# Performance work log

Hardware: AMD Instinct MI355X
Metric: run time of the kernel (lower is better)

The kernel has to match this reference:

```python
import jax, jax.numpy as jnp
import numpy as np

B, N, D_FEAT = 16, 1024, 64
NPOINT, RADIUS, NSAMPLE = 512, 0.2, 32
EPS = 1e-5


def _square_distance(src, dst):
    # src [b,S,3], dst [b,N,3] -> [b,S,N]
    d = -2.0 * jnp.einsum('bsc,bnc->bsn', src, dst)
    d = d + jnp.sum(src * src, -1)[:, :, None]
    d = d + jnp.sum(dst * dst, -1)[:, None, :]
    return d


def _fps(xyz, npoint):
    # xyz [b,N,3] -> indices [b,npoint]; seeded by point farthest from the mean
    b, n, _ = xyz.shape
    centroid = jnp.mean(xyz, axis=1, keepdims=True)
    distance = jnp.minimum(jnp.full((b, n), 1e10, xyz.dtype),
                           jnp.sum((xyz - centroid) ** 2, -1))
    farthest = jnp.argmax(distance, -1)
    bidx = jnp.arange(b)

    def body(carry, _):
        dist, far = carry
        c = xyz[bidx[:, None], far[:, None]]  # [b,1,3]
        dist = jnp.minimum(dist, jnp.sum((xyz - c) ** 2, -1))
        return (dist, jnp.argmax(dist, -1)), far

    _, idx = jax.lax.scan(body, (distance, farthest), None, length=npoint)
    return idx.T  # [b, npoint]


def _gather(points, idx):
    # points [b,N,C], idx [b,...] -> [b,...,C]
    return jax.vmap(lambda p, i: p[i])(points, idx)


def _query_ball(radius, nsample, xyz, new_xyz):
    # faithful to torch: mask out-of-radius with N, full sort, take first nsample,
    # replace sentinels by the first (closest-index) in-ball point
    b, n, _ = xyz.shape
    sqr = _square_distance(new_xyz, xyz)  # [b,S,N]
    idx = jnp.where(sqr > radius ** 2, n, jnp.arange(n)[None, None, :])
    idx = jnp.sort(idx, axis=-1)[:, :, :nsample]
    first = idx[:, :, :1]
    return jnp.where(idx == n, first, idx)


def _qbn(x):
    # QBN_RM training mode: divide by per-channel RMS of detached activations
    mean = jnp.mean(jax.lax.stop_gradient(x) ** 2, axis=(0, 2, 3))
    return x / jnp.sqrt(mean + EPS)[None, :, None, None]


def _qrelu(x):
    # scale each 3-vector by mod / max(mod, 1), coefficient detached
    b3, c, s, k = x.shape
    b = b3 // 3
    xd = jax.lax.stop_gradient(x).reshape(b, 3, c, s, k)
    mod = jnp.sqrt(jnp.sum(xd * xd, axis=1))  # [b,c,s,k]
    coeff = mod / jnp.maximum(mod, 1.0)
    return jnp.broadcast_to(coeff[:, None], (b, 3, c, s, k)).reshape(b3, c, s, k) * x


def _qmaxpool(x):
    # our_mpool1d with kernel (1, nsample): pick the max-modulus sample over K,
    # gather the same index for all 3 quaternion components
    b3, c, s, k = x.shape
    b = b3 // 3
    x5 = x.reshape(b, 3, c, s, k)
    mod = jnp.sum(jax.lax.stop_gradient(x5) ** 2, axis=1)  # argmax of mod == argmax of mod^2
    idx = jnp.argmax(mod, axis=-1)  # [b,c,s]
    idxb = jnp.broadcast_to(idx[:, None, :, :, None], (b, 3, c, s, 1))
    y = jnp.take_along_axis(x5, idxb, axis=-1)[..., 0]  # [b,3,c,s]
    return y.reshape(b3, c, s)


def setup_inputs() -> dict:
    key = jax.random.key(0)
    k1, k2, k3, k4, k5 = jax.random.split(key, 5)
    xyz = jax.random.normal(k1, (B, 3, N), dtype=jnp.float32)
    points = jax.random.normal(k2, (B * 3, D_FEAT, N), dtype=jnp.float32)
    W0 = jax.random.normal(k3, (64, 66), dtype=jnp.float32) * np.sqrt(2.0 / 66)
    W1 = jax.random.normal(k4, (64, 64), dtype=jnp.float32) * np.sqrt(2.0 / 64)
    W2 = jax.random.normal(k5, (128, 64), dtype=jnp.float32) * np.sqrt(2.0 / 64)
    return {"xyz": xyz, "points": points, "W0": W0, "W1": W1, "W2": W2}


def reference(xyz, points, W0, W1, W2):
    xyz_t = xyz.transpose(0, 2, 1)      # [B,N,3]
    pts_t = points.transpose(0, 2, 1)   # [B*3,N,D]

    fps_idx = _fps(xyz_t, NPOINT)                       # [B,S]
    new_xyz = _gather(xyz_t, fps_idx)                   # [B,S,3]
    idx = _query_ball(RADIUS, NSAMPLE, xyz_t, new_xyz)  # [B,S,K]

    g_xyz = _gather(xyz_t, idx)                         # [B,S,K,3]
    g_norm = g_xyz - new_xyz[:, :, None, :]
    gx = g_xyz.transpose(0, 3, 1, 2).reshape(B * 3, NPOINT, NSAMPLE, 1)
    gn = g_norm.transpose(0, 3, 1, 2).reshape(B * 3, NPOINT, NSAMPLE, 1)
    idx3 = jnp.broadcast_to(idx[:, None], (B, 3, NPOINT, NSAMPLE)).reshape(B * 3, NPOINT, NSAMPLE)
    gp = _gather(pts_t, idx3)                           # [B*3,S,K,D]

    x = jnp.concatenate([gn, gx, gp], axis=-1)          # [B*3,S,K,D+2]
    x = x.transpose(0, 3, 1, 2)                         # [B*3,D+2,S,K]
    for W in (W0, W1, W2):
        x = jnp.einsum('bcsk,oc->bosk', x, W)           # 1x1 conv, no bias
        x = _qrelu(_qbn(x))
    new_feat = _qmaxpool(x)                             # [B*3,128,S]
    return new_xyz.transpose(0, 2, 1), new_feat
```

## Files before the change

### kernel.cpp

```cpp
#include <hip/hip_runtime.h>

typedef unsigned int u32;
typedef unsigned long long u64;
typedef float v2f __attribute__((ext_vector_type(2)));

#define NB 16
#define NPT 1024
#define NP 512
#define NS 32
#define DF 64
#define RAD2 0.04f
#define EPSQ 1e-5f
#define CNTF 786432.0f
#define NGRP 8192
#define TCAP 96
#define TSLOT 128
#define NTILE_MAX 2731
#define NBALLBLK 4096
#define NFILLBLK 1366

__device__ __forceinline__ float rmul(float a, float b){ return __fmul_rn(a,b); }
__device__ __forceinline__ float radd(float a, float b){ return __fadd_rn(a,b); }
__device__ __forceinline__ float sq3(float a, float b, float c){
  return radd(radd(rmul(a,a), rmul(b,b)), rmul(c,c));
}

__device__ __forceinline__ float wave_sum64(float v){
  #pragma unroll
  for(int m=1;m<64;m<<=1) v += __shfl_xor(v, m, 64);
  return v;
}
__device__ __forceinline__ float half_sum32(float v){
  #pragma unroll
  for(int m=1;m<32;m<<=1) v += __shfl_xor(v, m, 64);
  return v;
}

#define DPPK(CTRL) do{ \
  unsigned _lo = (unsigned)k, _hi = (unsigned)(k>>32); \
  unsigned _mlo = (unsigned)__builtin_amdgcn_mov_dpp((int)_lo, (CTRL), 0xF, 0xF, true); \
  unsigned _mhi = (unsigned)__builtin_amdgcn_mov_dpp((int)_hi, (CTRL), 0xF, 0xF, true); \
  u64 _mk = ((u64)_mhi<<32) | _mlo; \
  k = (_mk > k) ? _mk : k; \
}while(0)

template<int PT>
__global__ __launch_bounds__(256, 1) void fps_combo(const float* __restrict__ xyz,
                                                    float* __restrict__ out0,
                                                    const float* __restrict__ pts,
                                                    float* __restrict__ ptsT,
                                                    u32* __restrict__ witem,
                                                    int* __restrict__ idxb_full,
                                                    int* __restrict__ cnt_full,
                                                    int* __restrict__ farIdx){
#pragma clang fp contract(off)
  const int bid = blockIdx.x;
  const int t = threadIdx.x;

  if(bid >= 8){
    if(bid < 8 + NBALLBLK){
      const int row = (bid - 8)*4 + (t>>6);
      const int lane = t & 63;
      const int b = row >> 10;
      const int nc = row & 1023;
      const float* xb = xyz + b*3*NPT;
      const float s0 = xb[nc], s1 = xb[NPT+nc], s2 = xb[2*NPT+nc];
      const float ss = sq3(s0,s1,s2);
      int base = 0;
      int* rowp = idxb_full + row*NS;
      for(int chk=0; chk<16 && base<NS; ++chk){
        const int n = chk*64 + lane;
        float d0 = xb[n], d1 = xb[NPT+n], d2 = xb[2*NPT+n];
        float dd = sq3(d0,d1,d2);
        float p  = radd(radd(rmul(s0,d0), rmul(s1,d1)), rmul(s2,d2));
        float sqr = radd(radd(rmul(-2.0f,p), ss), dd);
        bool inc = !(sqr > RAD2);
        u64 mask = __ballot(inc);
        if(inc){
          int slot = base + __popcll(mask & ((1ull<<lane)-1ull));
          if(slot < NS) rowp[slot] = n;
        }
        base += __popcll(mask);
      }
      if(lane==0) cnt_full[row] = (base < NS) ? base : NS;
    } else {
      const int gid = (bid - 8 - NBALLBLK)*256 + t;
      if(gid < NTILE_MAX*TSLOT) witem[gid] = 0xFFFFFFFFu;
      if constexpr(PT){
        const int w = gid >> 6, ln = gid & 63;
        if(w < 48*16){
          const int b3 = w >> 4, n0 = (w & 15) << 6;
          const float* src = pts + (((size_t)b3*64 + ln) << 10);
          float* dst = ptsT + (((size_t)b3*1024 + n0) << 6) + ln;
          #pragma unroll 4
          for(int i=0;i<64;i++) dst[(size_t)i << 6] = src[n0 + i];
        }
      }
    }
    return;
  }

  __shared__ float4 plds[2048];
  if(t >= 64) return;
  __builtin_amdgcn_s_setprio(3);
  const int lane = t;
  const int half = lane >> 5;
  const int hl   = lane & 31;
  const int b    = 2*bid + half;
  const float* xb = xyz + b*3*NPT;

  v2f px2[16], py2[16], pz2[16], dist2[16];
  u32 loj[32];
  #pragma unroll
  for(int i=0;i<16;i++){
    const int n0 = 64*i + hl, n1 = n0 + 32;
    float x0v = xb[n0],        x1v = xb[n1];
    float y0v = xb[NPT+n0],    y1v = xb[NPT+n1];
    float z0v = xb[2*NPT+n0],  z1v = xb[2*NPT+n1];
    px2[i].x = x0v; px2[i].y = x1v;
    py2[i].x = y0v; py2[i].y = y1v;
    pz2[i].x = z0v; pz2[i].y = z1v;
    loj[2*i]   = 1023u - (u32)n0;
    loj[2*i+1] = 1023u - (u32)n1;
    plds[(half<<10) + n0] = make_float4(x0v, y0v, z0v, 0.f);
    plds[(half<<10) + n1] = make_float4(x1v, y1v, z1v, 0.f);
  }
  float sx=0.f, sy=0.f, sz=0.f;
  #pragma unroll
  for(int i=0;i<16;i++){
    sx += px2[i].x; sx += px2[i].y;
    sy += py2[i].x; sy += py2[i].y;
    sz += pz2[i].x; sz += pz2[i].y;
  }
  sx = half_sum32(sx); sy = half_sum32(sy); sz = half_sum32(sz);
  const float cx = sx/1024.f, cy = sy/1024.f, cz = sz/1024.f;
  {
    v2f cx2; cx2.x=cx; cx2.y=cx;
    v2f cy2; cy2.x=cy; cy2.y=cy;
    v2f cz2; cz2.x=cz; cz2.y=cz;
    #pragma unroll
    for(int i=0;i<16;i++){
      v2f dx = px2[i]-cx2, dy = py2[i]-cy2, dz = pz2[i]-cz2;
      v2f m1 = dx*dx, m2 = dy*dy, a1 = m1+m2, m3 = dz*dz, s2 = a1+m3;
      dist2[i].x = fminf(1e10f, s2.x);
      dist2[i].y = fminf(1e10f, s2.y);
    }
  }
  auto reduce2 = [&](int& fA, int& fB){
    u64 kk[16];
    #pragma unroll
    for(int i=0;i<16;i++){
      float a = dist2[i].x, bb = dist2[i].y;
      bool tk = bb > a;
      float dw = tk ? bb : a;
      u32   lw = tk ? loj[2*i+1] : loj[2*i];
      kk[i] = ((u64)__float_as_uint(dw)<<32) | lw;
    }
    #pragma unroll
    for(int i=0;i<8;i++){ u64 l=kk[2*i], r=kk[2*i+1]; kk[i] = (r>l)?r:l; }
    #pragma unroll
    for(int i=0;i<4;i++){ u64 l=kk[2*i], r=kk[2*i+1]; kk[i] = (r>l)?r:l; }
    #pragma unroll
    for(int i=0;i<2;i++){ u64 l=kk[2*i], r=kk[2*i+1]; kk[i] = (r>l)?r:l; }
    u64 k = (kk[1]>kk[0]) ? kk[1] : kk[0];
    DPPK(0xB1); DPPK(0x4E); DPPK(0x124); DPPK(0x128); DPPK(0x142);
    unsigned lo = (unsigned)k;
    fA = 1023 - __builtin_amdgcn_readlane((int)lo, 31);
    fB = 1023 - __builtin_amdgcn_readlane((int)lo, 63);
  };

  __asm__ volatile("s_waitcnt lgkmcnt(0)" ::: "memory");
  int farA, farB;
  reduce2(farA, farB);
  for(int it=0; it<NP; ++it){
    const int farv = (lane & 32) ? farB : farA;
    const float4 qv = plds[(half<<10) + farv];
    if(hl == 0){
      out0[(b*3+0)*NP + it] = qv.x;
      out0[(b*3+1)*NP + it] = qv.y;
      out0[(b*3+2)*NP + it] = qv.z;
      farIdx[b*NP + it] = farv;
    }
    v2f qx2; qx2.x=qv.x; qx2.y=qv.x;
    v2f qy2; qy2.x=qv.y; qy2.y=qv.y;
    v2f qz2; qz2.x=qv.z; qz2.y=qv.z;
    #pragma unroll
    for(int i=0;i<16;i++){
      v2f dx = px2[i]-qx2, dy = py2[i]-qy2, dz = pz2[i]-qz2;
      v2f m1 = dx*dx, m2 = dy*dy, a1 = m1+m2, m3 = dz*dz, s2 = a1+m3;
      dist2[i].x = fminf(dist2[i].x, s2.x);
      dist2[i].y = fminf(dist2[i].y, s2.y);
    }
    reduce2(farA, farB);
  }
}

__global__ __launch_bounds__(1024) void pack_kernel(const int* __restrict__ farIdx,
                                                    const int* __restrict__ cnt_full,
                                                    const int* __restrict__ idxb_full,
                                                    u32* __restrict__ witem,
                                                    int* __restrict__ ntile_dev,
                                                    int* __restrict__ cntb){
  const int t = threadIdx.x;
  const int lane = t & 63;
  const int wv = t >> 6;
  int c[8]; int rowid[8]; int s0 = 0;
  #pragma unroll
  for(int i=0;i<8;i++){
    const int g = t*8+i;
    const int far = farIdx[g];
    rowid[i] = ((g>>9)<<10) + far;
    c[i] = cnt_full[rowid[i]];
    cntb[g] = c[i];
    s0 += c[i];
  }
  int pre = s0;
  #pragma unroll
  for(int d=1; d<64; d<<=1){
    int v = __shfl_up(pre, d, 64);
    if(lane >= d) pre += v;
  }
  __shared__ int wsum[16];
  if(lane==63) wsum[wv] = pre;
  __syncthreads();
  int wo = 0;
  #pragma unroll
  for(int w=0;w<16;w++) if(w < wv) wo += wsum[w];
  int m = wo + pre - s0;
  if(t==1023) *ntile_dev = (wo + pre + TCAP - 1) / TCAP;
  #pragma unroll
  for(int i=0;i<8;i++){
    const int g = t*8+i; const int cc = c[i];
    const int tile = m / TCAP; const int slot = m - TCAP*tile;
    const int* rp = idxb_full + rowid[i]*NS;
    for(int j=0;j<cc;j++){
      witem[tile*TSLOT + slot + j] = (u32)((g<<15) | (j<<10) | rp[j]);
    }
    m += cc;
  }
}

template<int DEPTH, int PT>
__global__ __launch_bounds__(384) void pass_kernel(
  const float* __restrict__ xyz, const float* __restrict__ ptsrc,
  const float* __restrict__ W0, const float* __restrict__ W1, const float* __restrict__ W2,
  const float* __restrict__ out0, const u32* __restrict__ witem,
  const int* __restrict__ cntb, const int* __restrict__ ntile_dev,
  const float* __restrict__ inv1, const float* __restrict__ inv2,
  float* __restrict__ part, float* __restrict__ out1,
  int cache_tiles, float* __restrict__ cacheA, float* __restrict__ cacheB)
{
  const int t = threadIdx.x;
  const int c3 = t >> 7;
  const int r  = t & 127;
  const int lane = t & 63;
  const int wv = t >> 6;
  const int bi = blockIdx.x;

  if(bi >= *ntile_dev) return;
  const bool use_cache = (bi < cache_tiles);
  float* cslotA = cacheA + ((size_t)bi*TSLOT + r)*192 + (size_t)c3*64;
  float* cslotB = cacheB + ((size_t)bi*TSLOT + r)*192 + (size_t)c3*64;

  __shared__ float sq[3][128][17];
  __shared__ float wstat[6][128];
  for(int i=t; i<6*128; i+=384) (&wstat[0][0])[i] = 0.f;
  __syncthreads();

  const u32 w = witem[bi*TSLOT + r];
  const bool valid = (w != 0xFFFFFFFFu);
  const int bs = valid ? (int)(w >> 15) : 0;
  const int j  = valid ? (int)((w >> 10) & 31) : 1;
  const int n  = valid ? (int)(w & 1023) : 0;
  const int b = bs >> 9;
  const int s = bs & 511;
  const int b3 = b*3 + c3;
  const int cv = cntb[bs];
  const float wgt = valid ? ((j==0) ? (float)(33 - cv) : 1.0f) : 0.0f;

  float acc2[64];
  const bool skip01 = (DEPTH == 3) && use_cache;

  if(!skip01){
    float acc64[64];
    if(DEPTH >= 2 && use_cache){
      #pragma unroll
      for(int q=0;q<16;q++){
        float4 v = ((const float4*)cslotA)[q];
        acc64[4*q]=v.x; acc64[4*q+1]=v.y; acc64[4*q+2]=v.z; acc64[4*q+3]=v.w;
      }
    } else {
      const float gx = xyz[b3*NPT + n];
      const float cx = out0[b3*NP + s];
      float x0[66];
      x0[0] = gx - cx;
      x0[1] = gx;
      if constexpr(PT){
        const float4* pr4 = reinterpret_cast<const float4*>(ptsrc + (((size_t)b3<<10) + (size_t)n)*DF);
        #pragma unroll
        for(int q=0;q<16;q++){
          float4 v = pr4[q];
          x0[2+4*q] = v.x; x0[3+4*q] = v.y; x0[4+4*q] = v.z; x0[5+4*q] = v.w;
        }
      } else {
        const float* pr = ptsrc + ((size_t)b3*DF)*NPT + n;
        #pragma unroll
        for(int c=0;c<DF;c++) x0[2+c] = pr[(size_t)c*NPT];
      }
      #pragma unroll
      for(int ch=0; ch<4; ++ch){
        #pragma unroll
        for(int oo=0;oo<16;oo++){
          const int o = ch*16+oo;
          float a = 0.f;
          #pragma unroll
          for(int c=0;c<66;c++) a = fmaf(W0[o*66+c], x0[c], a);
          acc64[o] = a;
        }
      }
      if(DEPTH == 1 && use_cache){
        #pragma unroll
        for(int q=0;q<16;q++){
          float4 v; v.x=acc64[4*q]; v.y=acc64[4*q+1]; v.z=acc64[4*q+2]; v.w=acc64[4*q+3];
          ((float4*)cslotA)[q] = v;
        }
      }
    }

    if constexpr(DEPTH == 1){
      #pragma unroll
      for(int o=0;o<64;o++){
        float v = wave_sum64(acc64[o]*acc64[o]*wgt);
        if(lane==0) wstat[wv][o] += v;
      }
      __syncthreads();
      if(t < 64){
        float sv = 0.f;
        #pragma unroll
        for(int wq=0;wq<6;wq++) sv += wstat[wq][t];
        part[bi*64 + t] = sv;
      }
      return;
    }

    float y1[64];
    #pragma unroll
    for(int ch=0; ch<4; ++ch){
      float xp16[16];
      #pragma unroll
      for(int oo=0;oo<16;oo++){
        const int o = ch*16+oo;
        float xp = acc64[o] * inv1[o];
        xp16[oo] = xp;
        sq[c3][r][oo] = xp*xp;
      }
      __syncthreads();
      #pragma unroll
      for(int oo=0;oo<16;oo++){
        float m2 = (sq[0][r][oo] + sq[1][r][oo]) + sq[2][r][oo];
        float mod = sqrtf(m2);
        float cf = (mod >= 1.f) ? 1.f : mod;
        y1[ch*16+oo] = cf * xp16[oo];
      }
      __syncthreads();
    }

    #pragma unroll
    for(int ch=0; ch<4; ++ch){
      #pragma unroll
      for(int oo=0;oo<16;oo++){
        const int o = ch*16+oo;
        float a = 0.f;
        #pragma unroll
        for(int c=0;c<64;c++) a = fmaf(W1[o*64+c], y1[c], a);
        acc2[o] = a;
      }
    }
    if(DEPTH == 2 && use_cache){
      #pragma unroll
      for(int q=0;q<16;q++){
        float4 v; v.x=acc2[4*q]; v.y=acc2[4*q+1]; v.z=acc2[4*q+2]; v.w=acc2[4*q+3];
        ((float4*)cslotB)[q] = v;
      }
    }
  } else {
    #pragma unroll
    for(int q=0;q<16;q++){
      float4 v = ((const float4*)cslotB)[q];
      acc2[4*q]=v.x; acc2[4*q+1]=v.y; acc2[4*q+2]=v.z; acc2[4*q+3]=v.w;
    }
  }

  if constexpr(DEPTH == 2){
    #pragma unroll
    for(int o=0;o<64;o++){
      float v = wave_sum64(acc2[o]*acc2[o]*wgt);
      if(lane==0) wstat[wv][o] += v;
    }
    __syncthreads();
    if(t < 64){
      float sv = 0.f;
      #pragma unroll
      for(int wq=0;wq<6;wq++) sv += wstat[wq][t];
      part[bi*64 + t] = sv;
    }
    return;
  }

  if constexpr(DEPTH == 3){
    float y2[64];
    #pragma unroll
    for(int ch=0; ch<4; ++ch){
      float xp16[16];
      #pragma unroll
      for(int oo=0;oo<16;oo++){
        const int o = ch*16+oo;
        float xp = acc2[o] * inv2[o];
        xp16[oo] = xp;
        sq[c3][r][oo] = xp*xp;
      }
      __syncthreads();
      #pragma unroll
      for(int oo=0;oo<16;oo++){
        float m2 = (sq[0][r][oo] + sq[1][r][oo]) + sq[2][r][oo];
        float mod = sqrtf(m2);
        float cf = (mod >= 1.f) ? 1.f : mod;
        y2[ch*16+oo] = cf * xp16[oo];
      }
      __syncthreads();
    }

    #pragma unroll
    for(int ch=0; ch<8; ++ch){
      #pragma unroll
      for(int oo=0;oo<16;oo++){
        const int o = ch*16+oo;
        float a = 0.f;
        #pragma unroll
        for(int c=0;c<64;c++) a = fmaf(W2[o*64+c], y2[c], a);
        sq[c3][r][oo] = a;
      }
      __syncthreads();
      if(c3 == 0){
        #pragma unroll
        for(int oo=0;oo<16;oo++){
          float a0 = sq[0][r][oo], a1 = sq[1][r][oo], a2 = sq[2][r][oo];
          float m2 = radd(radd(rmul(a0,a0), rmul(a1,a1)), rmul(a2,a2));
          float v = wave_sum64(m2*wgt);
          if(lane==0) wstat[wv][ch*16+oo] += v;
          if(valid && j==0){
            float bvv = m2; int bjj = 0;
            for(int jj=1; jj<cv; ++jj){
              float c0 = sq[0][r+jj][oo], c1 = sq[1][r+jj][oo], c2 = sq[2][r+jj][oo];
              float mm = radd(radd(rmul(c0,c0), rmul(c1,c1)), rmul(c2,c2));
              if(mm > bvv){ bvv = mm; bjj = jj; }
            }
            const int o = ch*16+oo;
            #pragma unroll
            for(int cc=0;cc<3;cc++){
              out1[(((size_t)(3*b+cc))*128 + o)*NP + s] = sq[cc][r+bjj][oo];
            }
          }
        }
      }
      __syncthreads();
    }
    if(t < 128){
      part[bi*128 + t] = wstat[0][t] + wstat[1][t];
    }
  }
}

__global__ __launch_bounds__(256) void fin_kernel(const float* __restrict__ part,
                                                  const int* __restrict__ ntile_dev, int nch,
                                                  float* __restrict__ inv){
  const int o = blockIdx.x;
  const int t = threadIdx.x;
  const int nblk = *ntile_dev;
  float sum = 0.f;
  for(int i=t; i<nblk; i+=256) sum += part[(size_t)i*nch + o];
  sum = wave_sum64(sum);
  __shared__ float red[4];
  if((t&63)==0) red[t>>6] = sum;
  __syncthreads();
  if(t==0){
    float tot = (red[0]+red[1])+(red[2]+red[3]);
    inv[o] = 1.0f / sqrtf(tot/CNTF + EPSQ);
  }
}

__global__ __launch_bounds__(256) void fin3_scale(const float* __restrict__ part3,
                                                  const int* __restrict__ ntile_dev,
                                                  float* __restrict__ out){
  const int o = blockIdx.x;
  const int t = threadIdx.x;
  const int nblk = *ntile_dev;
  float sum = 0.f;
  for(int i=t; i<nblk; i+=256) sum += part3[(size_t)i*128 + o];
  sum = wave_sum64(sum);
  __shared__ float red[4];
  __shared__ float sinv;
  if((t&63)==0) red[t>>6] = sum;
  __syncthreads();
  if(t==0){
    float tot = (red[0]+red[1])+(red[2]+red[3]);
    sinv = 1.0f / sqrtf(tot/CNTF + EPSQ);
  }
  __syncthreads();
  const float iv = sinv;
  float* base = out + NB*3*NP;
  const size_t str = (size_t)128*NP;
  for(int idx=t; idx<NB*NP; idx+=256){
    const int b = idx >> 9, s = idx & 511;
    size_t i0 = ((size_t)(b*3)*128 + o)*NP + s;
    float a0 = base[i0] * iv;
    float a1 = base[i0+str] * iv;
    float a2 = base[i0+2*str] * iv;
    float m2 = (a0*a0 + a1*a1) + a2*a2;
    float mod = sqrtf(m2);
    float cf = (mod >= 1.f) ? 1.f : mod;
    base[i0] = cf*a0; base[i0+str] = cf*a1; base[i0+2*str] = cf*a2;
  }
}

extern "C" void kernel_launch(void* const* d_in, const int* in_sizes, int n_in,
                              void* d_out, int out_size, void* d_ws, size_t ws_size,
                              hipStream_t stream){
  const float* xyz = (const float*)d_in[0];
  const float* pts = (const float*)d_in[1];
  const float* W0  = (const float*)d_in[2];
  const float* W1  = (const float*)d_in[3];
  const float* W2  = (const float*)d_in[4];
  float* out = (float*)d_out;

  char* p = (char*)d_ws;
  auto carve = [&](size_t bytes)->char*{
    char* q = p; p += (bytes + 255) & ~(size_t)255; return q;
  };
  int*   idxb_full = (int*)  carve((size_t)NB*NPT*NS*4);
  int*   cnt_full  = (int*)  carve((size_t)NB*NPT*4);
  int*   farIdx    = (int*)  carve((size_t)NGRP*4);
  int*   cntb      = (int*)  carve((size_t)NGRP*4);
  u32*   witem     = (u32*)  carve((size_t)NTILE_MAX*TSLOT*4);
  int*   ntile_dev = (int*)  carve(256);
  float* part1     = (float*)carve((size_t)NTILE_MAX*64*4);
  float* part2     = (float*)carve((size_t)NTILE_MAX*64*4);
  float* part3     = (float*)carve((size_t)NTILE_MAX*128*4);
  float* inv1      = (float*)carve(64*4);
  float* inv2      = (float*)carve(64*4);
  size_t base_need = (size_t)(p - (char*)d_ws);
  float* ptsT      = (float*)p;
  const size_t pt_bytes = (size_t)48*1024*64*4;
  const bool use_pt = (ws_size >= base_need + pt_bytes + (1u<<20));

  size_t fixed = base_need + (use_pt ? pt_bytes : 0);
  const size_t per_tile = (size_t)TSLOT*192*4*2;
  int cache_tiles = 0;
  if(ws_size > fixed + per_tile)
    cache_tiles = (int)((ws_size - fixed) / per_tile);
  if(cache_tiles > NTILE_MAX) cache_tiles = NTILE_MAX;
  float* cacheA = (float*)((char*)d_ws + fixed);
  float* cacheB = cacheA + (size_t)cache_tiles*TSLOT*192;

  float* out1 = out + NB*3*NP;
  const int nblk = 8 + NBALLBLK + NFILLBLK;

  if(use_pt) fps_combo<1><<<nblk, 256, 0, stream>>>(xyz, out, pts, ptsT, witem, idxb_full, cnt_full, farIdx);
  else       fps_combo<0><<<nblk, 256, 0, stream>>>(xyz, out, pts, nullptr, witem, idxb_full, cnt_full, farIdx);

  pack_kernel<<<1, 1024, 0, stream>>>(farIdx, cnt_full, idxb_full, witem, ntile_dev, cntb);

  if(use_pt){
    pass_kernel<1,1><<<NTILE_MAX, 384, 0, stream>>>(xyz, ptsT, W0, W1, W2, out, witem, cntb, ntile_dev, nullptr, nullptr, part1, nullptr, cache_tiles, cacheA, cacheB);
    fin_kernel<<<64, 256, 0, stream>>>(part1, ntile_dev, 64, inv1);
    pass_kernel<2,1><<<NTILE_MAX, 384, 0, stream>>>(xyz, ptsT, W0, W1, W2, out, witem, cntb, ntile_dev, inv1, nullptr, part2, nullptr, cache_tiles, cacheA, cacheB);
    fin_kernel<<<64, 256, 0, stream>>>(part2, ntile_dev, 64, inv2);
    pass_kernel<3,1><<<NTILE_MAX, 384, 0, stream>>>(xyz, ptsT, W0, W1, W2, out, witem, cntb, ntile_dev, inv1, inv2, part3, out1, cache_tiles, cacheA, cacheB);
  } else {
    pass_kernel<1,0><<<NTILE_MAX, 384, 0, stream>>>(xyz, pts, W0, W1, W2, out, witem, cntb, ntile_dev, nullptr, nullptr, part1, nullptr, cache_tiles, cacheA, cacheB);
    fin_kernel<<<64, 256, 0, stream>>>(part1, ntile_dev, 64, inv1);
    pass_kernel<2,0><<<NTILE_MAX, 384, 0, stream>>>(xyz, pts, W0, W1, W2, out, witem, cntb, ntile_dev, inv1, nullptr, part2, nullptr, cache_tiles, cacheA, cacheB);
    fin_kernel<<<64, 256, 0, stream>>>(part2, ntile_dev, 64, inv2);
    pass_kernel<3,0><<<NTILE_MAX, 384, 0, stream>>>(xyz, pts, W0, W1, W2, out, witem, cntb, ntile_dev, inv1, inv2, part3, out1, cache_tiles, cacheA, cacheB);
  }
  fin3_scale<<<128, 256, 0, stream>>>(part3, ntile_dev, out);
}
```

Before: 744.5 us.

## Fuse pack stage into FPS kernel via atomic completion flag; persistent pass grid

Removes the separate single-block pack kernel launch. An extra block is appended to the FPS/ball-query kernel that spins on a global atomic counter until all other blocks have signalled completion, then does the prefix-sum packing itself. The pass kernels also switch from one block per tile to a fixed 512-block grid that loops over tiles. The spin-wait relies on the last block being scheduled after the others and includes a timeout escape that could silently produce wrong results. A memset launch is added to reset the flag.

After: 958.6 us. 28.8% more time.

```diff
diff --git a/kernel.cpp b/kernel.cpp
--- a/kernel.cpp
+++ b/kernel.cpp
@@ -18,6 +18,8 @@
 #define NTILE_MAX 2731
 #define NBALLBLK 4096
 #define NFILLBLK 1366
+#define NSIG (8 + NBALLBLK + NFILLBLK)
+#define NPGRID 512
 
 __device__ __forceinline__ float rmul(float a, float b){ return __fmul_rn(a,b); }
 __device__ __forceinline__ float radd(float a, float b){ return __fadd_rn(a,b); }
@@ -43,6 +45,10 @@
   u64 _mk = ((u64)_mhi<<32) | _mlo; \
   k = (_mk > k) ? _mk : k; \
 }while(0)
+
+__device__ __forceinline__ void signal_done(int* flagp){
+  __hip_atomic_fetch_add(flagp, 1, __ATOMIC_RELEASE, __HIP_MEMORY_SCOPE_AGENT);
+}
 
 template<int PT>
 __global__ __launch_bounds__(256, 1) void fps_combo(const float* __restrict__ xyz,
@@ -52,10 +58,57 @@
                                                     u32* __restrict__ witem,
                                                     int* __restrict__ idxb_full,
                                                     int* __restrict__ cnt_full,
-                                                    int* __restrict__ farIdx){
+                                                    int* __restrict__ farIdx,
+                                                    int* __restrict__ cntb,
+                                                    int* __restrict__ ntile_dev,
+                                                    int* __restrict__ flagp){
 #pragma clang fp contract(off)
   const int bid = blockIdx.x;
   const int t = threadIdx.x;
+
+  if(bid == NSIG){
+    if(t == 0){
+      const u64 t0 = __builtin_amdgcn_s_memrealtime();
+      while(__hip_atomic_load(flagp, __ATOMIC_ACQUIRE, __HIP_MEMORY_SCOPE_AGENT) < NSIG){
+        __builtin_amdgcn_s_sleep(64);
+        if(__builtin_amdgcn_s_memrealtime() - t0 > 2000000ull) break;
+      }
+    }
+    __syncthreads();
+    __shared__ int tsum[256];
+    int s0 = 0;
+    for(int i=0;i<32;i++){
+      const int g = t*32+i;
+      const int far = farIdx[g];
+      const int rid = ((g>>9)<<10) + far;
+      const int cc = cnt_full[rid];
+      cntb[g] = cc;
+      s0 += cc;
+    }
+    tsum[t] = s0;
+    __syncthreads();
+    for(int ofs=1; ofs<256; ofs<<=1){
+      int v = (t >= ofs) ? tsum[t-ofs] : 0;
+      __syncthreads();
+      tsum[t] += v;
+      __syncthreads();
+    }
+    int m = tsum[t] - s0;
+    if(t==255) *ntile_dev = (tsum[255] + TCAP - 1) / TCAP;
+    for(int i=0;i<32;i++){
+      const int g = t*32+i;
+      const int far = farIdx[g];
+      const int rid = ((g>>9)<<10) + far;
+      const int cc = cntb[g];
+      const int tile = m / TCAP; const int slot = m - TCAP*tile;
+      const int* rp = idxb_full + rid*NS;
+      for(int j=0;j<cc;j++){
+        witem[tile*TSLOT + slot + j] = (u32)((g<<15) | (j<<10) | rp[j]);
+      }
+      m += cc;
+    }
+    return;
+  }
 
   if(bid >= 8){
     if(bid < 8 + NBALLBLK){
@@ -83,9 +136,13 @@
         base += __popcll(mask);
       }
       if(lane==0) cnt_full[row] = (base < NS) ? base : NS;
+      __syncthreads();
+      if(t==0) signal_done(flagp);
     } else {
       const int gid = (bid - 8 - NBALLBLK)*256 + t;
       if(gid < NTILE_MAX*TSLOT) witem[gid] = 0xFFFFFFFFu;
+      __syncthreads();
+      if(t==0) signal_done(flagp);
       if constexpr(PT){
         const int w = gid >> 6, ln = gid & 63;
         if(w < 48*16){
@@ -193,51 +250,8 @@
     }
     reduce2(farA, farB);
   }
-}
-
-__global__ __launch_bounds__(1024) void pack_kernel(const int* __restrict__ farIdx,
-                                                    const int* __restrict__ cnt_full,
-                                                    const int* __restrict__ idxb_full,
-                                                    u32* __restrict__ witem,
-                                                    int* __restrict__ ntile_dev,
-                                                    int* __restrict__ cntb){
-  const int t = threadIdx.x;
-  const int lane = t & 63;
-  const int wv = t >> 6;
-  int c[8]; int rowid[8]; int s0 = 0;
-  #pragma unroll
-  for(int i=0;i<8;i++){
-    const int g = t*8+i;
-    const int far = farIdx[g];
-    rowid[i] = ((g>>9)<<10) + far;
-    c[i] = cnt_full[rowid[i]];
-    cntb[g] = c[i];
-    s0 += c[i];
-  }
-  int pre = s0;
-  #pragma unroll
-  for(int d=1; d<64; d<<=1){
-    int v = __shfl_up(pre, d, 64);
-    if(lane >= d) pre += v;
-  }
-  __shared__ int wsum[16];
-  if(lane==63) wsum[wv] = pre;
-  __syncthreads();
-  int wo = 0;
-  #pragma unroll
-  for(int w=0;w<16;w++) if(w < wv) wo += wsum[w];
-  int m = wo + pre - s0;
-  if(t==1023) *ntile_dev = (wo + pre + TCAP - 1) / TCAP;
-  #pragma unroll
-  for(int i=0;i<8;i++){
-    const int g = t*8+i; const int cc = c[i];
-    const int tile = m / TCAP; const int slot = m - TCAP*tile;
-    const int* rp = idxb_full + rowid[i]*NS;
-    for(int j=0;j<cc;j++){
-      witem[tile*TSLOT + slot + j] = (u32)((g<<15) | (j<<10) | rp[j]);
-    }
-    m += cc;
-  }
+  __asm__ volatile("s_waitcnt vmcnt(0)" ::: "memory");
+  if(t == 0) signal_done(flagp);
 }
 
 template<int DEPTH, int PT>
@@ -255,58 +269,120 @@
   const int r  = t & 127;
   const int lane = t & 63;
   const int wv = t >> 6;
-  const int bi = blockIdx.x;
-
-  if(bi >= *ntile_dev) return;
-  const bool use_cache = (bi < cache_tiles);
-  float* cslotA = cacheA + ((size_t)bi*TSLOT + r)*192 + (size_t)c3*64;
-  float* cslotB = cacheB + ((size_t)bi*TSLOT + r)*192 + (size_t)c3*64;
+
+  const int ntile = *ntile_dev;
+  if(blockIdx.x >= ntile) return;
 
   __shared__ float sq[3][128][17];
   __shared__ float wstat[6][128];
-  for(int i=t; i<6*128; i+=384) (&wstat[0][0])[i] = 0.f;
-  __syncthreads();
-
-  const u32 w = witem[bi*TSLOT + r];
-  const bool valid = (w != 0xFFFFFFFFu);
-  const int bs = valid ? (int)(w >> 15) : 0;
-  const int j  = valid ? (int)((w >> 10) & 31) : 1;
-  const int n  = valid ? (int)(w & 1023) : 0;
-  const int b = bs >> 9;
-  const int s = bs & 511;
-  const int b3 = b*3 + c3;
-  const int cv = cntb[bs];
-  const float wgt = valid ? ((j==0) ? (float)(33 - cv) : 1.0f) : 0.0f;
-
-  float acc2[64];
-  const bool skip01 = (DEPTH == 3) && use_cache;
-
-  if(!skip01){
-    float acc64[64];
-    if(DEPTH >= 2 && use_cache){
+
+  for(int bi = blockIdx.x; bi < ntile; bi += NPGRID){
+    const bool use_cache = (bi < cache_tiles);
+    float* cslotA = cacheA + ((size_t)bi*TSLOT + r)*192 + (size_t)c3*64;
+    float* cslotB = cacheB + ((size_t)bi*TSLOT + r)*192 + (size_t)c3*64;
+
+    for(int i=t; i<6*128; i+=384) (&wstat[0][0])[i] = 0.f;
+    __syncthreads();
+
+    const u32 w = witem[bi*TSLOT + r];
+    const bool valid = (w != 0xFFFFFFFFu);
+    const int bs = valid ? (int)(w >> 15) : 0;
+    const int j  = valid ? (int)((w >> 10) & 31) : 1;
+    const int n  = valid ? (int)(w & 1023) : 0;
+    const int b = bs >> 9;
+    const int s = bs & 511;
+    const int b3 = b*3 + c3;
+    const int cv = cntb[bs];
+    const float wgt = valid ? ((j==0) ? (float)(33 - cv) : 1.0f) : 0.0f;
+
+    float acc2[64];
+    const bool skip01 = (DEPTH == 3) && use_cache;
+
+    if(!skip01){
+      float acc64[64];
+      if(DEPTH >= 2 && use_cache){
+        #pragma unroll
+        for(int q=0;q<16;q++){
+          float4 v = ((const float4*)cslotA)[q];
+          acc64[4*q]=v.x; acc64[4*q+1]=v.y; acc64[4*q+2]=v.z; acc64[4*q+3]=v.w;
+        }
+      } else {
+        const float gx = xyz[b3*NPT + n];
+        const float cx = out0[b3*NP + s];
+        float x0[66];
+        x0[0] = gx - cx;
+        x0[1] = gx;
+        if constexpr(PT){
+          const float4* pr4 = reinterpret_cast<const float4*>(ptsrc + (((size_t)b3<<10) + (size_t)n)*DF);
+          #pragma unroll
+          for(int q=0;q<16;q++){
+            float4 v = pr4[q];
+            x0[2+4*q] = v.x; x0[3+4*q] = v.y; x0[4+4*q] = v.z; x0[5+4*q] = v.w;
+          }
+        } else {
+          const float* pr = ptsrc + ((size_t)b3*DF)*NPT + n;
+          #pragma unroll
+          for(int c=0;c<DF;c++) x0[2+c] = pr[(size_t)c*NPT];
+        }
+        #pragma unroll
+        for(int ch=0; ch<4; ++ch){
+          #pragma unroll
+          for(int oo=0;oo<16;oo++){
+            const int o = ch*16+oo;
+            float a = 0.f;
+            #pragma unroll
+            for(int c=0;c<66;c++) a = fmaf(W0[o*66+c], x0[c], a);
+            acc64[o] = a;
+          }
+        }
+        if(DEPTH == 1 && use_cache){
+          #pragma unroll
+          for(int q=0;q<16;q++){
+            float4 v; v.x=acc64[4*q]; v.y=acc64[4*q+1]; v.z=acc64[4*q+2]; v.w=acc64[4*q+3];
+            ((float4*)cslotA)[q] = v;
+          }
+        }
+      }
+
+      if constexpr(DEPTH == 1){
+        #pragma unroll
+        for(int o=0;o<64;o++){
+          float v = wave_sum64(acc64[o]*acc64[o]*wgt);
+          if(lane==0) wstat[wv][o] += v;
+        }
+        __syncthreads();
+        if(t < 64){
+          float sv = 0.f;
+          #pragma unroll
+          for(int wq=0;wq<6;wq++) sv += wstat[wq][t];
+          part[bi*64 + t] = sv;
+        }
+        __syncthreads();
+        continue;
+      }
+
+      float y1[64];
       #pragma unroll
-      for(int q=0;q<16;q++){
-        float4 v = ((const float4*)cslotA)[q];
-        acc64[4*q]=v.x; acc64[4*q+1]=v.y; acc64[4*q+2]=v.z; acc64[4*q+3]=v.w;
-      }
-    } else {
-      const float gx = xyz[b3*NPT + n];
-      const float cx = out0[b3*NP + s];
-      float x0[66];
-      x0[0] = gx - cx;
-      x0[1] = gx;
-      if constexpr(PT){
-        const float4* pr4 = reinterpret_cast<const float4*>(ptsrc + (((size_t)b3<<10) + (size_t)n)*DF);
-        #pragma unroll
-        for(int q=0;q<16;q++){
-          float4 v = pr4[q];
-          x0[2+4*q] = v.x; x0[3+4*q] = v.y; x0[4+4*q] = v.z; x0[5+4*q] = v.w;
-        }
-      } else {
-        const float* pr = ptsrc + ((size_t)b3*DF)*NPT + n;
-        #pragma unroll
-        for(int c=0;c<DF;c++) x0[2+c] = pr[(size_t)c*NPT];
-      }
+      for(int ch=0; ch<4; ++ch){
+        float xp16[16];
+        #pragma unroll
+        for(int oo=0;oo<16;oo++){
+          const int o = ch*16+oo;
+          float xp = acc64[o] * inv1[o];
+          xp16[oo] = xp;
+          sq[c3][r][oo] = xp*xp;
+        }
+        __syncthreads();
+        #pragma unroll
+        for(int oo=0;oo<16;oo++){
+          float m2 = (sq[0][r][oo] + sq[1][r][oo]) + sq[2][r][oo];
+          float mod = sqrtf(m2);
+          float cf = (mod >= 1.f) ? 1.f : mod;
+          y1[ch*16+oo] = cf * xp16[oo];
+        }
+        __syncthreads();
+      }
+
       #pragma unroll
       for(int ch=0; ch<4; ++ch){
         #pragma unroll
@@ -314,23 +390,29 @@
           const int o = ch*16+oo;
           float a = 0.f;
           #pragma unroll
-          for(int c=0;c<66;c++) a = fmaf(W0[o*66+c], x0[c], a);
-          acc64[o] = a;
-        }
-      }
-      if(DEPTH == 1 && use_cache){
+          for(int c=0;c<64;c++) a = fmaf(W1[o*64+c], y1[c], a);
+          acc2[o] = a;
+        }
+      }
+      if(DEPTH == 2 && use_cache){
         #pragma unroll
         for(int q=0;q<16;q++){
-          float4 v; v.x=acc64[4*q]; v.y=acc64[4*q+1]; v.z=acc64[4*q+2]; v.w=acc64[4*q+3];
-          ((float4*)cslotA)[q] = v;
-        }
-      }
-    }
-
-    if constexpr(DEPTH == 1){
+          float4 v; v.x=acc2[4*q]; v.y=acc2[4*q+1]; v.z=acc2[4*q+2]; v.w=acc2[4*q+3];
+          ((float4*)cslotB)[q] = v;
+        }
+      }
+    } else {
+      #pragma unroll
+      for(int q=0;q<16;q++){
+        float4 v = ((const float4*)cslotB)[q];
+        acc2[4*q]=v.x; acc2[4*q+1]=v.y; acc2[4*q+2]=v.z; acc2[4*q+3]=v.w;
+      }
+    }
+
+    if constexpr(DEPTH == 2){
       #pragma unroll
       for(int o=0;o<64;o++){
-        float v = wave_sum64(acc64[o]*acc64[o]*wgt);
+        float v = wave_sum64(acc2[o]*acc2[o]*wgt);
         if(lane==0) wstat[wv][o] += v;
       }
       __syncthreads();
@@ -340,133 +422,72 @@
         for(int wq=0;wq<6;wq++) sv += wstat[wq][t];
         part[bi*64 + t] = sv;
       }
-      return;
-    }
-
-    float y1[64];
-    #pragma unroll
-    for(int ch=0; ch<4; ++ch){
-      float xp16[16];
+      __syncthreads();
+      continue;
+    }
+
+    if constexpr(DEPTH == 3){
+      float y2[64];
       #pragma unroll
-      for(int oo=0;oo<16;oo++){
-        const int o = ch*16+oo;
-        float xp = acc64[o] * inv1[o];
-        xp16[oo] = xp;
-        sq[c3][r][oo] = xp*xp;
-      }
-      __syncthreads();
+      for(int ch=0; ch<4; ++ch){
+        float xp16[16];
+        #pragma unroll
+        for(int oo=0;oo<16;oo++){
+          const int o = ch*16+oo;
+          float xp = acc2[o] * inv2[o];
+          xp16[oo] = xp;
+          sq[c3][r][oo] = xp*xp;
+        }
+        __syncthreads();
+        #pragma unroll
+        for(int oo=0;oo<16;oo++){
+          float m2 = (sq[0][r][oo] + sq[1][r][oo]) + sq[2][r][oo];
+          float mod = sqrtf(m2);
+          float cf = (mod >= 1.f) ? 1.f : mod;
+          y2[ch*16+oo] = cf * xp16[oo];
+        }
+        __syncthreads();
+      }
+
       #pragma unroll
-      for(int oo=0;oo<16;oo++){
-        float m2 = (sq[0][r][oo] + sq[1][r][oo]) + sq[2][r][oo];
-        float mod = sqrtf(m2);
-        float cf = (mod >= 1.f) ? 1.f : mod;
-        y1[ch*16+oo] = cf * xp16[oo];
-      }
-      __syncthreads();
-    }
-
-    #pragma unroll
-    for(int ch=0; ch<4; ++ch){
-      #pragma unroll
-      for(int oo=0;oo<16;oo++){
-        const int o = ch*16+oo;
-        float a = 0.f;
-        #pragma unroll
-        for(int c=0;c<64;c++) a = fmaf(W1[o*64+c], y1[c], a);
-        acc2[o] = a;
-      }
-    }
-    if(DEPTH == 2 && use_cache){
-      #pragma unroll
-      for(int q=0;q<16;q++){
-        float4 v; v.x=acc2[4*q]; v.y=acc2[4*q+1]; v.z=acc2[4*q+2]; v.w=acc2[4*q+3];
-        ((float4*)cslotB)[q] = v;
-      }
-    }
-  } else {
-    #pragma unroll
-    for(int q=0;q<16;q++){
-      float4 v = ((const float4*)cslotB)[q];
-      acc2[4*q]=v.x; acc2[4*q+1]=v.y; acc2[4*q+2]=v.z; acc2[4*q+3]=v.w;
-    }
-  }
-
-  if constexpr(DEPTH == 2){
-    #pragma unroll
-    for(int o=0;o<64;o++){
-      float v = wave_sum64(acc2[o]*acc2[o]*wgt);
-      if(lane==0) wstat[wv][o] += v;
-    }
-    __syncthreads();
-    if(t < 64){
-      float sv = 0.f;
-      #pragma unroll
-      for(int wq=0;wq<6;wq++) sv += wstat[wq][t];
-      part[bi*64 + t] = sv;
-    }
-    return;
-  }
-
-  if constexpr(DEPTH == 3){
-    float y2[64];
-    #pragma unroll
-    for(int ch=0; ch<4; ++ch){
-      float xp16[16];
-      #pragma unroll
-      for(int oo=0;oo<16;oo++){
-        const int o = ch*16+oo;
-        float xp = acc2[o] * inv2[o];
-        xp16[oo] = xp;
-        sq[c3][r][oo] = xp*xp;
-      }
-      __syncthreads();
-      #pragma unroll
-      for(int oo=0;oo<16;oo++){
-        float m2 = (sq[0][r][oo] + sq[1][r][oo]) + sq[2][r][oo];
-        float mod = sqrtf(m2);
-        float cf = (mod >= 1.f) ? 1.f : mod;
-        y2[ch*16+oo] = cf * xp16[oo];
-      }
-      __syncthreads();
-    }
-
-    #pragma unroll
-    for(int ch=0; ch<8; ++ch){
-      #pragma unroll
-      for(int oo=0;oo<16;oo++){
-        const int o = ch*16+oo;
-        float a = 0.f;
-        #pragma unroll
-        for(int c=0;c<64;c++) a = fmaf(W2[o*64+c], y2[c], a);
-        sq[c3][r][oo] = a;
-      }
-      __syncthreads();
-      if(c3 == 0){
+      for(int ch=0; ch<8; ++ch){
         #pragma unroll
         for(int oo=0;oo<16;oo++){
-          float a0 = sq[0][r][oo], a1 = sq[1][r][oo], a2 = sq[2][r][oo];
-          float m2 = radd(radd(rmul(a0,a0), rmul(a1,a1)), rmul(a2,a2));
-          float v = wave_sum64(m2*wgt);
-          if(lane==0) wstat[wv][ch*16+oo] += v;
-          if(valid && j==0){
-            float bvv = m2; int bjj = 0;
-            for(int jj=1; jj<cv; ++jj){
-              float c0 = sq[0][r+jj][oo], c1 = sq[1][r+jj][oo], c2 = sq[2][r+jj][oo];
-              float mm = radd(radd(rmul(c0,c0), rmul(c1,c1)), rmul(c2,c2));
-              if(mm > bvv){ bvv = mm; bjj = jj; }
-            }
-            const int o = ch*16+oo;
-            #pragma unroll
-            for(int cc=0;cc<3;cc++){
-              out1[(((size_t)(3*b+cc))*128 + o)*NP + s] = sq[cc][r+bjj][oo];
+          const int o = ch*16+oo;
+          float a = 0.f;
+          #pragma unroll
+          for(int c=0;c<64;c++) a = fmaf(W2[o*64+c], y2[c], a);
+          sq[c3][r][oo] = a;
+        }
+        __syncthreads();
+        if(c3 == 0){
+          #pragma unroll
+          for(int oo=0;oo<16;oo++){
+            float a0 = sq[0][r][oo], a1 = sq[1][r][oo], a2 = sq[2][r][oo];
+            float m2 = radd(radd(rmul(a0,a0), rmul(a1,a1)), rmul(a2,a2));
+            float v = wave_sum64(m2*wgt);
+            if(lane==0) wstat[wv][ch*16+oo] += v;
+            if(valid && j==0){
+              float bvv = m2; int bjj = 0;
+              for(int jj=1; jj<cv; ++jj){
+                float c0 = sq[0][r+jj][oo], c1 = sq[1][r+jj][oo], c2 = sq[2][r+jj][oo];
+                float mm = radd(radd(rmul(c0,c0), rmul(c1,c1)), rmul(c2,c2));
+                if(mm > bvv){ bvv = mm; bjj = jj; }
+              }
+              const int o = ch*16+oo;
+              #pragma unroll
+              for(int cc=0;cc<3;cc++){
+                out1[(((size_t)(3*b+cc))*128 + o)*NP + s] = sq[cc][r+bjj][oo];
+              }
             }
           }
         }
+        __syncthreads();
+      }
+      if(t < 128){
+        part[bi*128 + t] = wstat[0][t] + wstat[1][t];
       }
       __syncthreads();
-    }
-    if(t < 128){
-      part[bi*128 + t] = wstat[0][t] + wstat[1][t];
     }
   }
 }
@@ -543,6 +564,7 @@
   int*   cntb      = (int*)  carve((size_t)NGRP*4);
   u32*   witem     = (u32*)  carve((size_t)NTILE_MAX*TSLOT*4);
   int*   ntile_dev = (int*)  carve(256);
+  int*   flagp     = (int*)  carve(256);
   float* part1     = (float*)carve((size_t)NTILE_MAX*64*4);
   float* part2     = (float*)carve((size_t)NTILE_MAX*64*4);
   float* part3     = (float*)carve((size_t)NTILE_MAX*128*4);
@@ -563,25 +585,24 @@
   float* cacheB = cacheA + (size_t)cache_tiles*TSLOT*192;
 
   float* out1 = out + NB*3*NP;
-  const int nblk = 8 + NBALLBLK + NFILLBLK;
-
-  if(use_pt) fps_combo<1><<<nblk, 256, 0, stream>>>(xyz, out, pts, ptsT, witem, idxb_full, cnt_full, farIdx);
-  else       fps_combo<0><<<nblk, 256, 0, stream>>>(xyz, out, pts, nullptr, witem, idxb_full, cnt_full, farIdx);
-
-  pack_kernel<<<1, 1024, 0, stream>>>(farIdx, cnt_full, idxb_full, witem, ntile_dev, cntb);
+  const int nblk = NSIG + 1;
+
+  hipMemsetAsync(flagp, 0, 4, stream);
+  if(use_pt) fps_combo<1><<<nblk, 256, 0, stream>>>(xyz, out, pts, ptsT, witem, idxb_full, cnt_full, farIdx, cntb, ntile_dev, flagp);
+  else       fps_combo<0><<<nblk, 256, 0, stream>>>(xyz, out, pts, nullptr, witem, idxb_full, cnt_full, farIdx, cntb, ntile_dev, flagp);
 
   if(use_pt){
-    pass_kernel<1,1><<<NTILE_MAX, 384, 0, stream>>>(xyz, ptsT, W0, W1, W2, out, witem, cntb, ntile_dev, nullptr, nullptr, part1, nullptr, cache_tiles, cacheA, cacheB);
+    pass_kernel<1,1><<<NPGRID, 384, 0, stream>>>(xyz, ptsT, W0, W1, W2, out, witem, cntb, ntile_dev, nullptr, nullptr, part1, nullptr, cache_tiles, cacheA, cacheB);
     fin_kernel<<<64, 256, 0, stream>>>(part1, ntile_dev, 64, inv1);
-    pass_kernel<2,1><<<NTILE_MAX, 384, 0, stream>>>(xyz, ptsT, W0, W1, W2, out, witem, cntb, ntile_dev, inv1, nullptr, part2, nullptr, cache_tiles, cacheA, cacheB);
+    pass_kernel<2,1><<<NPGRID, 384, 0, stream>>>(xyz, ptsT, W0, W1, W2, out, witem, cntb, ntile_dev, inv1, nullptr, part2, nullptr, cache_tiles, cacheA, cacheB);
     fin_kernel<<<64, 256, 0, stream>>>(part2, ntile_dev, 64, inv2);
-    pass_kernel<3,1><<<NTILE_MAX, 384, 0, stream>>>(xyz, ptsT, W0, W1, W2, out, witem, cntb, ntile_dev, inv1, inv2, part3, out1, cache_tiles, cacheA, cacheB);
+    pass_kernel<3,1><<<NPGRID, 384, 0, stream>>>(xyz, ptsT, W0, W1, W2, out, witem, cntb, ntile_dev, inv1, inv2, part3, out1, cache_tiles, cacheA, cacheB);
   } else {
-    pass_kernel<1,0><<<NTILE_MAX, 384, 0, stream>>>(xyz, pts, W0, W1, W2, out, witem, cntb, ntile_dev, nullptr, nullptr, part1, nullptr, cache_tiles, cacheA, cacheB);
+    pass_kernel<1,0><<<NPGRID, 384, 0, stream>>>(xyz, pts, W0, W1, W2, out, witem, cntb, ntile_dev, nullptr, nullptr, part1, nullptr, cache_tiles, cacheA, cacheB);
     fin_kernel<<<64, 256, 0, stream>>>(part1, ntile_dev, 64, inv1);
-    pass_kernel<2,0><<<NTILE_MAX, 384, 0, stream>>>(xyz, pts, W0, W1, W2, out, witem, cntb, ntile_dev, inv1, nullptr, part2, nullptr, cache_tiles, cacheA, cacheB);
+    pass_kernel<2,0><<<NPGRID, 384, 0, stream>>>(xyz, pts, W0, W1, W2, out, witem, cntb, ntile_dev, inv1, nullptr, part2, nullptr, cache_tiles, cacheA, cacheB);
     fin_kernel<<<64, 256, 0, stream>>>(part2, ntile_dev, 64, inv2);
-    pass_kernel<3,0><<<NTILE_MAX, 384, 0, stream>>>(xyz, pts, W0, W1, W2, out, witem, cntb, ntile_dev, inv1, inv2, part3, out1, cache_tiles, cacheA, cacheB);
+    pass_kernel<3,0><<<NPGRID, 384, 0, stream>>>(xyz, pts, W0, W1, W2, out, witem, cntb, ntile_dev, inv1, inv2, part3, out1, cache_tiles, cacheA, cacheB);
   }
   fin3_scale<<<128, 256, 0, stream>>>(part3, ntile_dev, out);
 }
```
